# Kernel optimization log

Hardware: AMD Instinct MI355X
Metric: run time of the kernel (lower is better)

The kernel has to match this reference:

```python
import jax, jax.numpy as jnp
import numpy as np

TEMPERATURE = 0.07
B, D = 8192, 256

def _l2norm(x, axis=-1, eps=1e-12):
    # matches torch F.normalize(p=2): x / max(||x||, eps)
    n = jnp.sqrt(jnp.sum(x * x, axis=axis, keepdims=True))
    return x / jnp.maximum(n, eps)

def setup_inputs() -> dict:
    key = jax.random.key(0)
    k1, k2, k3 = jax.random.split(key, 3)
    return {
        "h_emb": jax.random.normal(k1, (B, D), dtype=jnp.float32),
        "r_emb": jax.random.normal(k2, (B, D), dtype=jnp.float32),
        "t_emb": jax.random.normal(k3, (B, D), dtype=jnp.float32),
    }

def reference(h_emb, r_emb, t_emb):
    # query = normalize(h + r); positives/negatives = normalize(t)
    q = _l2norm(h_emb + r_emb, axis=1)          # [B, D]
    t = _l2norm(t_emb, axis=1)                  # [B, D]
    # Dense in-batch similarity. The original builds logits = [pos, off-diag negs];
    # since the diagonal of sim IS the positive similarity, cross-entropy with
    # label 0 equals logsumexp over the full row minus the diagonal entry.
    sim = jnp.einsum('bd,nd->bn', q, t) / TEMPERATURE   # [B, B]
    pos = jnp.diagonal(sim)                              # [B]
    loss = jnp.mean(jax.nn.logsumexp(sim, axis=1) - pos)
    return loss
```

## Files before the change

kernel.cpp:

```cpp
#include <hip/hip_runtime.h>
#include <hip/hip_bf16.h>

#define B_DIM 8192
#define D_DIM 256
#define GRID_GEMM 512
#define NT 16

constexpr float INV_T = 14.285714285714286f;

typedef __bf16 bf16x8 __attribute__((ext_vector_type(8)));
typedef float  f32x16 __attribute__((ext_vector_type(16)));

#define GLOBAL_U32(p) ((const __attribute__((address_space(1))) unsigned int*)(p))
#define LDS_U32(p)    ((__attribute__((address_space(3))) unsigned int*)(p))

__device__ inline unsigned short f2bf(float f) {
    union { float f; unsigned u; } x; x.f = f;
    unsigned r = x.u + 0x7fffu + ((x.u >> 16) & 1u);
    return (unsigned short)(r >> 16);
}

__global__ __launch_bounds__(256) void norm_kernel(
    const float* __restrict__ h, const float* __restrict__ r,
    const float* __restrict__ t,
    unsigned short* __restrict__ qws, unsigned short* __restrict__ tws,
    float* __restrict__ rowsum, float* __restrict__ diagsum, int* __restrict__ ticket)
{
    if (blockIdx.x == 0) {
        float4* rs4 = (float4*)rowsum;
#pragma unroll
        for (int i = 0; i < 8; ++i)
            rs4[threadIdx.x * 8 + i] = make_float4(0.f, 0.f, 0.f, 0.f);
        if (threadIdx.x == 0) { *diagsum = 0.f; *ticket = 0; }
    }

    int wave = threadIdx.x >> 6;
    int lane = threadIdx.x & 63;
    int task = blockIdx.x * 4 + wave;
    bool isQ = task < B_DIM;
    int row  = isQ ? task : task - B_DIM;

    float4 v;
    if (isQ) {
        float4 a = ((const float4*)h)[row * 64 + lane];
        float4 b = ((const float4*)r)[row * 64 + lane];
        v = make_float4(a.x + b.x, a.y + b.y, a.z + b.z, a.w + b.w);
    } else {
        v = ((const float4*)t)[row * 64 + lane];
    }
    float s = v.x * v.x + v.y * v.y + v.z * v.z + v.w * v.w;
#pragma unroll
    for (int off = 32; off; off >>= 1) s += __shfl_xor(s, off, 64);
    float scale = 1.0f / fmaxf(sqrtf(s), 1e-12f);

    ushort4 o;
    o.x = f2bf(v.x * scale);
    o.y = f2bf(v.y * scale);
    o.z = f2bf(v.z * scale);
    o.w = f2bf(v.w * scale);
    ushort4* dst = (ushort4*)(isQ ? qws : tws);
    dst[row * 64 + lane] = o;
}

__global__ __launch_bounds__(256, 2) void gemm_lse_kernel(
    const unsigned char* __restrict__ qws, const unsigned char* __restrict__ tws,
    float* __restrict__ rowsum, float* __restrict__ diagsum,
    int* __restrict__ ticket, float* __restrict__ out)
{
    __shared__ __align__(16) unsigned char ldsB[2][64 * 512];
    __shared__ float wred[4];
    __shared__ int lastflag;

    const int tid  = threadIdx.x;
    const int lane = tid & 63;
    const int w    = tid >> 6;
    const int l31  = lane & 31;
    const int hi   = lane >> 5;
    const int wm   = w >> 1;
    const int wn   = w & 1;

    const int rb   = blockIdx.x & 63;
    const int cc   = blockIdx.x >> 6;
    const int row0 = rb * 128 + wm * 64;
    const int col0 = cc * 1024;

    bf16x8 a[2][16];
    {
        const unsigned char* abase = qws + (size_t)(row0 + l31) * 512 + hi * 16;
#pragma unroll
        for (int rt = 0; rt < 2; ++rt)
#pragma unroll
            for (int ks = 0; ks < 16; ++ks)
                a[rt][ks] = *(const bf16x8*)(abase + rt * (32 * 512) + ks * 32);
    }

    int srel[8];
#pragma unroll
    for (int it = 0; it < 8; ++it) {
        int s = it * 256 + tid;
        int n = s >> 5;
        int kc = (s & 31) ^ (n & 7);
        srel[it] = n * 512 + kc * 16;
    }
    const unsigned char* bSrc = tws + (size_t)col0 * 512;

    f32x16 rowacc[2] = {};
    float diagacc = 0.f;

#pragma unroll
    for (int it = 0; it < 8; ++it)
        __builtin_amdgcn_global_load_lds(GLOBAL_U32(bSrc + srel[it]),
                                         LDS_U32(&ldsB[0][(it * 256 + tid) * 16]),
                                         16, 0, 0);

    for (int nt = 0; nt < NT; ++nt) {
        const int cur = nt & 1;
        __syncthreads();

        if (nt + 1 < NT) {
            const unsigned char* gs = bSrc + (nt + 1) * 64 * 512;
#pragma unroll
            for (int it = 0; it < 8; ++it)
                __builtin_amdgcn_global_load_lds(
                    GLOBAL_U32(gs + srel[it]),
                    LDS_U32(&ldsB[cur ^ 1][(it * 256 + tid) * 16]), 16, 0, 0);
        }

        const unsigned char* bbuf = ldsB[cur];
        const int nloc = wn * 32 + l31;
        const int nsw  = nloc & 7;
        f32x16 acc0 = {}, acc1 = {};
#pragma unroll
        for (int ks = 0; ks < 16; ++ks) {
            int kc = ks * 2 + hi;
            bf16x8 b = *(const bf16x8*)(bbuf + nloc * 512 + ((kc ^ nsw) * 16));
            acc0 = __builtin_amdgcn_mfma_f32_32x32x16_bf16(a[0][ks], b, acc0, 0, 0, 0);
            acc1 = __builtin_amdgcn_mfma_f32_32x32x16_bf16(a[1][ks], b, acc1, 0, 0, 0);
        }

        const int coltile = col0 + nt * 64 + wn * 32;
        const bool isd0 = (row0 == coltile);
        const bool isd1 = (row0 + 32 == coltile);
#pragma unroll
        for (int g = 0; g < 16; ++g) {
            float d0 = acc0[g], d1 = acc1[g];
            rowacc[0][g] += __expf(fmaf(d0, INV_T, -INV_T));
            rowacc[1][g] += __expf(fmaf(d1, INV_T, -INV_T));
            int rm = (g & 3) + 8 * (g >> 2) + 4 * hi;
            if (isd0 && l31 == rm) diagacc += d0 * INV_T;
            if (isd1 && l31 == rm) diagacc += d1 * INV_T;
        }
    }

#pragma unroll
    for (int rt = 0; rt < 2; ++rt)
#pragma unroll
        for (int g = 0; g < 16; ++g) {
            float s = rowacc[rt][g];
            s += __shfl_xor(s, 1, 64);
            s += __shfl_xor(s, 2, 64);
            s += __shfl_xor(s, 4, 64);
            s += __shfl_xor(s, 8, 64);
            s += __shfl_xor(s, 16, 64);
            if (l31 == 0) {
                int grow = row0 + rt * 32 + (g & 3) + 8 * (g >> 2) + 4 * hi;
                atomicAdd(&rowsum[grow], s);
            }
        }

    float dsum = diagacc;
#pragma unroll
    for (int off = 32; off; off >>= 1) dsum += __shfl_xor(dsum, off, 64);
    if (lane == 0 && dsum != 0.f) atomicAdd(diagsum, dsum);

    __syncthreads();
    if (tid == 0) {
        __threadfence();
        int old = __hip_atomic_fetch_add(ticket, 1, __ATOMIC_ACQ_REL,
                                         __HIP_MEMORY_SCOPE_AGENT);
        lastflag = (old == GRID_GEMM - 1);
    }
    __syncthreads();
    if (!lastflag) return;

    float lsum = 0.f;
    for (int rr = tid; rr < B_DIM; rr += 256) {
        float rs = __hip_atomic_load(&rowsum[rr], __ATOMIC_RELAXED,
                                     __HIP_MEMORY_SCOPE_AGENT);
        lsum += __logf(rs);
    }
#pragma unroll
    for (int off = 32; off; off >>= 1) lsum += __shfl_xor(lsum, off, 64);
    if (lane == 0) wred[w] = lsum;
    __syncthreads();
    if (tid == 0) {
        float ds = __hip_atomic_load(diagsum, __ATOMIC_RELAXED,
                                     __HIP_MEMORY_SCOPE_AGENT);
        float total = wred[0] + wred[1] + wred[2] + wred[3]
                    + (float)B_DIM * INV_T
                    - ds;
        out[0] = total / (float)B_DIM;
    }
}

extern "C" void kernel_launch(void* const* d_in, const int* in_sizes, int n_in,
                              void* d_out, int out_size, void* d_ws, size_t ws_size,
                              hipStream_t stream)
{
    const float* h = (const float*)d_in[0];
    const float* r = (const float*)d_in[1];
    const float* t = (const float*)d_in[2];

    unsigned char* ws = (unsigned char*)d_ws;
    unsigned short* qws = (unsigned short*)ws;
    unsigned short* tws = (unsigned short*)(ws + 4u * 1024 * 1024);
    float* rowsum  = (float*)(ws + 8u * 1024 * 1024);
    float* diagsum = (float*)(ws + 8u * 1024 * 1024 + 32u * 1024);
    int*   ticket  = (int*)  (ws + 8u * 1024 * 1024 + 32u * 1024 + 16);

    norm_kernel<<<4096, 256, 0, stream>>>(h, r, t, qws, tws, rowsum, diagsum, ticket);
    gemm_lse_kernel<<<GRID_GEMM, 256, 0, stream>>>(
        (const unsigned char*)qws, (const unsigned char*)tws,
        rowsum, diagsum, ticket, (float*)d_out);
}
```

Baseline: 137.7 us.

## Use 4-deep LDS ring buffer with vmcnt waits and retile GEMM blocks

Changes the block tile from 128 rows x 1024 cols to 256 rows x 512 cols, with each wave owning 64 rows and sharing a 32-column B tile. Replaces the double buffer and per-iteration __syncthreads with a 4-slot LDS ring. Loads are prefetched two tiles ahead, and each iteration does a manual s_waitcnt vmcnt(8) plus a bare s_barrier. The aim is to hide global-to-LDS latency better and avoid draining all outstanding loads every iteration. The diagonal-extraction branch is also hoisted out of the exp loop. The costs are redundant tail loads and a delicate waitcnt encoding that correctness depends on.

New measurement: 132.5 us. 3.8% less time.

```diff
diff --git a/kernel.cpp b/kernel.cpp
--- a/kernel.cpp
+++ b/kernel.cpp
@@ -13,6 +13,8 @@
 
 #define GLOBAL_U32(p) ((const __attribute__((address_space(1))) unsigned int*)(p))
 #define LDS_U32(p)    ((__attribute__((address_space(3))) unsigned int*)(p))
+
+#define WAITCNT_VM8 0x0F78
 
 __device__ inline unsigned short f2bf(float f) {
     union { float f; unsigned u; } x; x.f = f;
@@ -67,7 +69,7 @@
     float* __restrict__ rowsum, float* __restrict__ diagsum,
     int* __restrict__ ticket, float* __restrict__ out)
 {
-    __shared__ __align__(16) unsigned char ldsB[2][64 * 512];
+    __shared__ __align__(16) unsigned char ldsB[4][32 * 512];
     __shared__ float wred[4];
     __shared__ int lastflag;
 
@@ -76,79 +78,85 @@
     const int w    = tid >> 6;
     const int l31  = lane & 31;
     const int hi   = lane >> 5;
-    const int wm   = w >> 1;
-    const int wn   = w & 1;
-
-    const int rb   = blockIdx.x & 63;
-    const int cc   = blockIdx.x >> 6;
-    const int row0 = rb * 128 + wm * 64;
-    const int col0 = cc * 1024;
-
-    bf16x8 a[2][16];
-    {
-        const unsigned char* abase = qws + (size_t)(row0 + l31) * 512 + hi * 16;
-#pragma unroll
-        for (int rt = 0; rt < 2; ++rt)
-#pragma unroll
-            for (int ks = 0; ks < 16; ++ks)
-                a[rt][ks] = *(const bf16x8*)(abase + rt * (32 * 512) + ks * 32);
-    }
-
-    int srel[8];
-#pragma unroll
-    for (int it = 0; it < 8; ++it) {
+
+    const int cc   = blockIdx.x & 15;
+    const int rb   = blockIdx.x >> 4;
+    const int row0 = rb * 256 + w * 64;
+    const int col0 = cc * 512;
+
+    int srel[4];
+#pragma unroll
+    for (int it = 0; it < 4; ++it) {
         int s = it * 256 + tid;
         int n = s >> 5;
         int kc = (s & 31) ^ (n & 7);
         srel[it] = n * 512 + kc * 16;
     }
-    const unsigned char* bSrc = tws + (size_t)col0 * 512;
+
+#define STAGE(snt, bufi)                                                     \
+    {                                                                        \
+        const unsigned char* gs = tws + (size_t)(col0 + (snt) * 32) * 512;   \
+        _Pragma("unroll")                                                    \
+        for (int it = 0; it < 4; ++it)                                       \
+            __builtin_amdgcn_global_load_lds(                                \
+                GLOBAL_U32(gs + srel[it]),                                   \
+                LDS_U32(&ldsB[bufi][(it * 256 + tid) * 16]), 16, 0, 0);      \
+    }
+
+    STAGE(0, 0);
+    STAGE(1, 1);
+
+    bf16x8 a[2][16];
+    {
+        const unsigned char* abase = qws + (size_t)(row0 + l31) * 512 + hi * 16;
+#pragma unroll
+        for (int rt = 0; rt < 2; ++rt)
+#pragma unroll
+            for (int ks = 0; ks < 16; ++ks)
+                a[rt][ks] = *(const bf16x8*)(abase + rt * (32 * 512) + ks * 32);
+    }
 
     f32x16 rowacc[2] = {};
     float diagacc = 0.f;
-
-#pragma unroll
-    for (int it = 0; it < 8; ++it)
-        __builtin_amdgcn_global_load_lds(GLOBAL_U32(bSrc + srel[it]),
-                                         LDS_U32(&ldsB[0][(it * 256 + tid) * 16]),
-                                         16, 0, 0);
+    const int nsw = l31 & 7;
 
     for (int nt = 0; nt < NT; ++nt) {
-        const int cur = nt & 1;
-        __syncthreads();
-
-        if (nt + 1 < NT) {
-            const unsigned char* gs = bSrc + (nt + 1) * 64 * 512;
-#pragma unroll
-            for (int it = 0; it < 8; ++it)
-                __builtin_amdgcn_global_load_lds(
-                    GLOBAL_U32(gs + srel[it]),
-                    LDS_U32(&ldsB[cur ^ 1][(it * 256 + tid) * 16]), 16, 0, 0);
-        }
-
-        const unsigned char* bbuf = ldsB[cur];
-        const int nloc = wn * 32 + l31;
-        const int nsw  = nloc & 7;
+        const int snt = (nt + 2 < NT) ? nt + 2 : NT - 1;
+        STAGE(snt, (nt + 2) & 3);
+
+        __builtin_amdgcn_s_waitcnt(WAITCNT_VM8);
+        __builtin_amdgcn_s_barrier();
+
+        const unsigned char* bbuf = ldsB[nt & 3];
         f32x16 acc0 = {}, acc1 = {};
 #pragma unroll
         for (int ks = 0; ks < 16; ++ks) {
             int kc = ks * 2 + hi;
-            bf16x8 b = *(const bf16x8*)(bbuf + nloc * 512 + ((kc ^ nsw) * 16));
+            bf16x8 b = *(const bf16x8*)(bbuf + l31 * 512 + ((kc ^ nsw) * 16));
             acc0 = __builtin_amdgcn_mfma_f32_32x32x16_bf16(a[0][ks], b, acc0, 0, 0, 0);
             acc1 = __builtin_amdgcn_mfma_f32_32x32x16_bf16(a[1][ks], b, acc1, 0, 0, 0);
         }
 
-        const int coltile = col0 + nt * 64 + wn * 32;
-        const bool isd0 = (row0 == coltile);
-        const bool isd1 = (row0 + 32 == coltile);
 #pragma unroll
         for (int g = 0; g < 16; ++g) {
-            float d0 = acc0[g], d1 = acc1[g];
-            rowacc[0][g] += __expf(fmaf(d0, INV_T, -INV_T));
-            rowacc[1][g] += __expf(fmaf(d1, INV_T, -INV_T));
-            int rm = (g & 3) + 8 * (g >> 2) + 4 * hi;
-            if (isd0 && l31 == rm) diagacc += d0 * INV_T;
-            if (isd1 && l31 == rm) diagacc += d1 * INV_T;
+            rowacc[0][g] += __expf(fmaf(acc0[g], INV_T, -INV_T));
+            rowacc[1][g] += __expf(fmaf(acc1[g], INV_T, -INV_T));
+        }
+
+        const int c0t = col0 + nt * 32;
+        if (c0t == row0) {
+#pragma unroll
+            for (int g = 0; g < 16; ++g) {
+                int rm = (g & 3) + 8 * (g >> 2) + 4 * hi;
+                if (l31 == rm) diagacc += acc0[g] * INV_T;
+            }
+        }
+        if (c0t == row0 + 32) {
+#pragma unroll
+            for (int g = 0; g < 16; ++g) {
+                int rm = (g & 3) + 8 * (g >> 2) + 4 * hi;
+                if (l31 == rm) diagacc += acc1[g] * INV_T;
+            }
         }
     }
 
```
